# Kernel optimization log

Measured on AMD Instinct MI355X. Metric: run time of the kernel, lower is better.

Reference implementation:

```python
import jax, jax.numpy as jnp
import numpy as np

B, NUM_VN, NUM_CN, D = 4, 65536, 32768, 32
DEG = 8
E = NUM_CN * DEG  # 262144 edges per side
HID, MSG = 40, 20


def setup_inputs() -> dict:
    key = jax.random.key(0)
    ks = jax.random.split(key, 16)
    inp = {
        "h_from": jax.random.normal(ks[0], (B, NUM_VN, D), jnp.float32),
        "h_to_x": jax.random.normal(ks[1], (B, NUM_CN, D), jnp.float32),
        "h_to_z": jax.random.normal(ks[2], (B, NUM_CN, D), jnp.float32),
        "hx_logit": jax.random.normal(ks[3], (B, NUM_CN), jnp.float32),
        "hz_logit": jax.random.normal(ks[4], (B, NUM_CN), jnp.float32),
        "from_ind_x": jax.random.randint(ks[5], (E,), 0, NUM_VN, jnp.int32),
        "to_ind_x": jax.random.randint(ks[6], (E,), 0, NUM_CN, jnp.int32),
        "from_ind_z": jax.random.randint(ks[7], (E,), 0, NUM_VN, jnp.int32),
        "to_ind_z": jax.random.randint(ks[8], (E,), 0, NUM_CN, jnp.int32),
        # msg MLP: in 2*D -> HID -> MSG ; embed MLP: in MSG+D+1 -> HID -> D
        "Wm1_x": jax.random.normal(ks[9], (2 * D, HID), jnp.float32) * 0.1,
        "Wm2_x": jax.random.normal(ks[10], (HID, MSG), jnp.float32) * 0.1,
        "Wm1_z": jax.random.normal(ks[11], (2 * D, HID), jnp.float32) * 0.1,
        "Wm2_z": jax.random.normal(ks[12], (HID, MSG), jnp.float32) * 0.1,
        "We1_x": jax.random.normal(ks[13], (MSG + D + 1, HID), jnp.float32) * 0.1,
        "We2_x": jax.random.normal(ks[14], (HID, D), jnp.float32) * 0.1,
        "We1_z": jax.random.normal(ks[15], (MSG + D + 1, HID), jnp.float32) * 0.1,
        "We2_z": jax.random.normal(jax.random.fold_in(key, 99), (HID, D), jnp.float32) * 0.1,
    }
    return inp


def _side(h_from, h_to, logit, from_ind, to_ind, Wm1, Wm2, We1, We2):
    # gather edge endpoint embeddings: [B, E, 2*D]
    feat = jnp.concatenate([h_from[:, from_ind], h_to[:, to_ind]], axis=-1)
    # per-edge message MLP (relu hidden, linear out, no bias): [B, E, MSG]
    msg = jax.nn.relu(feat @ Wm1) @ Wm2
    # segment-sum aggregation onto receiving check nodes: [B, NUM_CN, MSG]
    n_cn = h_to.shape[1]
    m = jnp.zeros((h_to.shape[0], n_cn, msg.shape[-1]), msg.dtype).at[:, to_ind].add(msg)
    # embedding update MLP on [m, h_to, logit]: [B, NUM_CN, D]
    emb_in = jnp.concatenate([m, h_to, logit[..., None]], axis=-1)
    return jax.nn.relu(emb_in @ We1) @ We2


def reference(h_from, h_to_x, h_to_z, hx_logit, hz_logit,
              from_ind_x, to_ind_x, from_ind_z, to_ind_z,
              Wm1_x, Wm2_x, Wm1_z, Wm2_z, We1_x, We2_x, We1_z, We2_z):
    h_to_x_new = _side(h_from, h_to_x, hx_logit, from_ind_x, to_ind_x,
                       Wm1_x, Wm2_x, We1_x, We2_x)
    h_to_z_new = _side(h_from, h_to_z, hz_logit, from_ind_z, to_ind_z,
                       Wm1_z, Wm2_z, We1_z, We2_z)
    return (h_to_x_new, h_to_z_new)
```

## Files before the change

### kernel.cpp

```cpp
#include <hip/hip_runtime.h>

#define NVN 65536
#define NCN 32768
#define NB 4
#define DIM 32
#define NE 262144
#define HID 40
#define MSGD 20
#define SLOT 40

typedef unsigned short u16;
typedef unsigned int u32;
typedef __attribute__((ext_vector_type(8))) short bf16x8;
typedef __attribute__((ext_vector_type(4))) float f32x4;

__device__ __forceinline__ u16 f2bf(float f) {
    u32 u = __float_as_uint(f);
    u += 0x7fff + ((u >> 16) & 1);
    return (u16)(u >> 16);
}
__device__ __forceinline__ float bflo(u32 u) { return __uint_as_float(u << 16); }
__device__ __forceinline__ float bfhi(u32 u) { return __uint_as_float(u & 0xffff0000u); }
__device__ __forceinline__ u32 pk2(float a, float b) {
    return (u32)f2bf(a) | ((u32)f2bf(b) << 16);
}


__global__ __launch_bounds__(256) void scatter_slot(const int* __restrict__ to_x,
                                                    const int* __restrict__ from_x,
                                                    const int* __restrict__ to_z,
                                                    const int* __restrict__ from_z,
                                                    int* __restrict__ cnt_x,
                                                    int* __restrict__ cnt_z,
                                                    u16* __restrict__ ef_x,
                                                    u16* __restrict__ ef_z) {
    int bid = blockIdx.x;
    int e = (bid & 1023) * 256 + threadIdx.x;
    const int* t; const int* f; int* cnt; u16* ef;
    if (bid < 1024) { t = to_x; f = from_x; cnt = cnt_x; ef = ef_x; }
    else            { t = to_z; f = from_z; cnt = cnt_z; ef = ef_z; }
    int c = t[e];
    int pos = atomicAdd(&cnt[c], 1);
    if (pos < SLOT) ef[c * SLOT + pos] = (u16)f[e];
}


__global__ __launch_bounds__(256) void precomp_mfma(
        const float* __restrict__ h_x, const float* __restrict__ h_z,
        const float* __restrict__ W_x, const float* __restrict__ W_z,
        u16* __restrict__ dst_x, u16* __restrict__ dst_z,
        int nrows) {
    __shared__ __attribute__((aligned(16))) u16 sA[128 * 32];
    __shared__ __attribute__((aligned(16))) u16 sB[32 * 48];
    __shared__ __attribute__((aligned(16))) u16 sOut[128 * 40];

    int bps = nrows >> 5;
    int bid = blockIdx.x;
    int side = bid / bps;
    int v0 = (bid - side * bps) << 5;

    const float* __restrict__ h = side ? h_z : h_x;
    const float* __restrict__ W = side ? W_z : W_x;
    u16* dst = side ? dst_z : dst_x;

    int tid = threadIdx.x;

    for (int i = tid; i < 32 * 48; i += 256) {
        int row = i / 48, col = i - row * 48;
        sB[i] = (col < 40) ? f2bf(W[row * 40 + col]) : (u16)0;
    }
    {
        int r = tid >> 1, p = tid & 1;
        int b = r >> 5, vloc = r & 31;
        const float4* hp = (const float4*)(h + ((size_t)b * nrows + v0 + vloc) * DIM + p * 16);
        float4 x0 = hp[0], x1 = hp[1], x2 = hp[2], x3 = hp[3];
        uint4* d = (uint4*)(sA + r * 32 + p * 16);
        d[0] = make_uint4(pk2(x0.x, x0.y), pk2(x0.z, x0.w), pk2(x1.x, x1.y), pk2(x1.z, x1.w));
        d[1] = make_uint4(pk2(x2.x, x2.y), pk2(x2.z, x2.w), pk2(x3.x, x3.y), pk2(x3.z, x3.w));
    }
    __syncthreads();

    int wid = tid >> 6;
    int lane = tid & 63;
    int li = lane & 15;
    int lk = lane >> 4;

    bf16x8 bfr[3];
#pragma unroll
    for (int jt = 0; jt < 3; jt++) {
        bf16x8 v;
#pragma unroll
        for (int rr = 0; rr < 8; rr++)
            v[rr] = (short)sB[(lk * 8 + rr) * 48 + jt * 16 + li];
        bfr[jt] = v;
    }

#pragma unroll
    for (int rt = 0; rt < 2; rt++) {
        int rowloc = wid * 32 + rt * 16;
        bf16x8 a = *(const bf16x8*)(sA + (rowloc + li) * 32 + lk * 8);
#pragma unroll
        for (int jt = 0; jt < 3; jt++) {
            f32x4 acc = {0.f, 0.f, 0.f, 0.f};
            acc = __builtin_amdgcn_mfma_f32_16x16x32_bf16(a, bfr[jt], acc, 0, 0, 0);
            int col = jt * 16 + li;
            if (col < 40) {
#pragma unroll
                for (int rr = 0; rr < 4; rr++)
                    sOut[(rowloc + lk * 4 + rr) * 40 + col] = f2bf(acc[rr]);
            }
        }
    }
    __syncthreads();

    {
        const u32* so = (const u32*)sOut;
        uint4* dp = (uint4*)((char*)dst + (size_t)v0 * 320);
        for (int i = tid; i < 640; i += 256) {
            int vloc = i / 20;
            int q0 = (i - vloc * 20) * 4;
            u32 vals[4];
#pragma unroll
            for (int j = 0; j < 4; j++) {
                int q = q0 + j;
                int ch, cp;
                if (q < 32)      { ch = q >> 2;        cp = (ch >> 2) * 10 + (q & 3); }
                else if (q < 64) { int t = q - 32; ch = t >> 2; cp = (ch >> 2) * 10 + 4 + (t & 3); }
                else             { int t = q - 64; ch = t >> 1; cp = (ch >> 2) * 10 + 8 + (t & 1); }
                int m = (ch & 3) * 32 + vloc;
                vals[j] = so[m * 20 + cp];
            }
            dp[i] = make_uint4(vals[0], vals[1], vals[2], vals[3]);
        }
    }
}


__global__ __launch_bounds__(256) void prepW(
        const float* __restrict__ Wm2_x, const float* __restrict__ Wm2_z,
        const float* __restrict__ We1_x, const float* __restrict__ We1_z,
        const float* __restrict__ We2_x, const float* __restrict__ We2_z,
        u16* __restrict__ BW_x, u16* __restrict__ BW_z,
        u16* __restrict__ W2_x, u16* __restrict__ W2_z) {
    int side = blockIdx.x;
    const float* Wm2 = side ? Wm2_z : Wm2_x;
    const float* We1 = side ? We1_z : We1_x;
    const float* We2 = side ? We2_z : We2_x;
    u16* BW = side ? BW_z : BW_x;
    u16* W2 = side ? W2_z : W2_x;
    int tid = threadIdx.x;
    for (int i = tid; i < 96 * 48; i += 256) {
        int row = i / 48, col = i % 48;
        float v = 0.f;
        if (col < 40) {
            if (row < 40) {
                for (int k = 0; k < MSGD; k++) v += Wm2[row * MSGD + k] * We1[k * HID + col];
            } else if (row < 72) {
                v = We1[(MSGD + row - 40) * HID + col];
            } else if (row == 72) {
                v = We1[(MSGD + DIM) * HID + col];
            }
        }
        BW[i] = f2bf(v);
    }
    for (int i = tid; i < 64 * 32; i += 256) {
        int row = i / 32, col = i % 32;
        W2[i] = (row < 40) ? f2bf(We2[row * 32 + col]) : (u16)0;
    }
}


__global__ __launch_bounds__(256, 8) void aggA_kernel(
        const u16* __restrict__ U2h_x, const u16* __restrict__ U2h_z,
        u16* __restrict__ ts_x, u16* __restrict__ ts_z,
        const int* __restrict__ cnt_x, const int* __restrict__ cnt_z,
        const u16* __restrict__ ef_x, const u16* __restrict__ ef_z) {
    int side = blockIdx.x >> 10;
    const char* Ubase = (const char*)(side ? U2h_z : U2h_x);
    char* ts = (char*)(side ? ts_z : ts_x);
    const int* cnt = side ? cnt_z : cnt_x;
    const u16* ef = side ? ef_z : ef_x;

    int gt = (blockIdx.x & 1023) * 256 + threadIdx.x;
    int c = gt >> 3;
    int l8 = gt & 7;
    int off16a = l8 * 16;
    int off8c = 256 + l8 * 8;

    char* tline = ts + (size_t)c * 320;
    uint4 T0 = *(const uint4*)(tline + off16a);
    uint4 T1 = *(const uint4*)(tline + off16a + 128);
    uint2 Tc = *(const uint2*)(tline + off8c);

    float s[20];
#pragma unroll
    for (int k = 0; k < 20; k++) s[k] = 0.f;

    int cn = cnt[c];
    cn = (cn < SLOT) ? cn : SLOT;
    const u16* efc = ef + c * SLOT;

    int vA = (cn > 0) ? (int)efc[0] : 0;
#define ACC(su, aw, tw) { \
    s[su]     += fmaxf(bflo(aw) + bflo(tw), 0.f); \
    s[(su)+1] += fmaxf(bfhi(aw) + bfhi(tw), 0.f); }
    for (int i = 0; i < cn; ++i) {
        const char* pa = Ubase + (size_t)vA * 320;
        uint4 A0 = *(const uint4*)(pa + off16a);
        uint4 A1 = *(const uint4*)(pa + off16a + 128);
        uint2 A2 = *(const uint2*)(pa + off8c);
        vA = (i + 1 < cn) ? (int)efc[i + 1] : 0;
        ACC(0, A0.x, T0.x)  ACC(2, A0.y, T0.y)  ACC(4, A0.z, T0.z)  ACC(6, A0.w, T0.w)
        ACC(8, A1.x, T1.x)  ACC(10, A1.y, T1.y) ACC(12, A1.z, T1.z) ACC(14, A1.w, T1.w)
        ACC(16, A2.x, Tc.x) ACC(18, A2.y, Tc.y)
    }
#undef ACC

    u32 sp[10];
#pragma unroll
    for (int jq = 0; jq < 5; jq++) {
        sp[2 * jq]     = pk2(s[4 * jq + 0], s[4 * jq + 1]);
        sp[2 * jq + 1] = pk2(s[4 * jq + 2], s[4 * jq + 3]);
    }
    *(uint4*)(tline + off16a)       = make_uint4(sp[0], sp[1], sp[2], sp[3]);
    *(uint4*)(tline + off16a + 128) = make_uint4(sp[4], sp[5], sp[6], sp[7]);
    *(uint2*)(tline + off8c)        = make_uint2(sp[8], sp[9]);
}


__global__ __launch_bounds__(256) void aggB_mfma(
        const u16* __restrict__ ts_x, const u16* __restrict__ ts_z,
        const float* __restrict__ h_to_x, const float* __restrict__ h_to_z,
        const float* __restrict__ logit_x, const float* __restrict__ logit_z,
        const u16* __restrict__ BW_x, const u16* __restrict__ BW_z,
        const u16* __restrict__ W2_x, const u16* __restrict__ W2_z,
        float* __restrict__ out) {
    __shared__ __attribute__((aligned(16))) u16 sA[128 * 96];
    __shared__ __attribute__((aligned(16))) u16 sH[128 * 64];
    __shared__ __attribute__((aligned(16))) u16 sBW[96 * 48];
    __shared__ __attribute__((aligned(16))) u16 sW2[64 * 32];

    int bid = blockIdx.x;
    int side = bid >> 10;
    const u16* ts = side ? ts_z : ts_x;
    const float* h_to = side ? h_to_z : h_to_x;
    const float* logit = side ? logit_z : logit_x;
    const u16* BWg = side ? BW_z : BW_x;
    const u16* W2g = side ? W2_z : W2_x;

    int tid = threadIdx.x;
    int rho0 = (bid & 1023) * 128;
    int b = rho0 >> 15;
    int c0 = rho0 & 32767;

    for (int i = tid; i < (96 * 48) / 8; i += 256)
        ((uint4*)sBW)[i] = ((const uint4*)BWg)[i];
    if (tid < (64 * 32) / 8) ((uint4*)sW2)[tid] = ((const uint4*)W2g)[tid];

    {
        int r = tid >> 1;
        int part = tid & 1;
        int c = c0 + r;
        char* srow = (char*)sA + r * 192;
        if (part == 0) {
            const char* tr = (const char*)ts + (size_t)c * 320;
            uint4 p0 = *(const uint4*)(tr + b * 16);
            uint4 p1 = *(const uint4*)(tr + 128 + b * 16);
            uint2 p2 = *(const uint2*)(tr + 256 + b * 8);
            uint4 p3 = *(const uint4*)(tr + (4 + b) * 16);
            uint4 p4 = *(const uint4*)(tr + 128 + (4 + b) * 16);
            uint2 p5 = *(const uint2*)(tr + 256 + (4 + b) * 8);
            *(uint4*)(srow + 0)  = p0;
            *(uint4*)(srow + 16) = p1;
            *(uint2*)(srow + 32) = p2;
            *(uint2*)(srow + 40) = make_uint2(p3.x, p3.y);
            *(uint2*)(srow + 48) = make_uint2(p3.z, p3.w);
            *(uint2*)(srow + 56) = make_uint2(p4.x, p4.y);
            *(uint2*)(srow + 64) = make_uint2(p4.z, p4.w);
            *(uint2*)(srow + 72) = p5;
            char* hrow = (char*)sH + r * 128;
            *(uint4*)(hrow + 96)  = make_uint4(0, 0, 0, 0);
            *(uint4*)(hrow + 112) = make_uint4(0, 0, 0, 0);
        } else {
            const float4* xp = (const float4*)(h_to + ((size_t)b * NCN + c) * DIM);
#pragma unroll
            for (int q = 0; q < 4; q++) {
                float4 x0 = xp[2 * q], x1 = xp[2 * q + 1];
                *(uint4*)(srow + 80 + q * 16) =
                    make_uint4(pk2(x0.x, x0.y), pk2(x0.z, x0.w),
                               pk2(x1.x, x1.y), pk2(x1.z, x1.w));
            }
            float lg = logit[(size_t)b * NCN + c];
            *(uint4*)(srow + 144) = make_uint4((u32)f2bf(lg), 0, 0, 0);
            *(uint4*)(srow + 160) = make_uint4(0, 0, 0, 0);
            *(uint4*)(srow + 176) = make_uint4(0, 0, 0, 0);
        }
    }
    __syncthreads();

    int wid = tid >> 6;
    int lane = tid & 63;
    int li = lane & 15;
    int lk = lane >> 4;
    int rowq = lk * 4;

    bf16x8 bA[3][3];
#pragma unroll
    for (int jt = 0; jt < 3; jt++)
#pragma unroll
        for (int ks = 0; ks < 3; ks++) {
            bf16x8 v;
#pragma unroll
            for (int rr = 0; rr < 8; rr++)
                v[rr] = (short)sBW[(ks * 32 + lk * 8 + rr) * 48 + jt * 16 + li];
            bA[jt][ks] = v;
        }

#pragma unroll
    for (int rt = 0; rt < 2; rt++) {
        int rowloc = wid * 32 + rt * 16;
        const char* abase = (const char*)sA + (rowloc + li) * 192 + lk * 16;
        bf16x8 a0 = *(const bf16x8*)(abase);
        bf16x8 a1 = *(const bf16x8*)(abase + 64);
        bf16x8 a2 = *(const bf16x8*)(abase + 128);
#pragma unroll
        for (int jt = 0; jt < 3; jt++) {
            f32x4 acc = {0.f, 0.f, 0.f, 0.f};
            acc = __builtin_amdgcn_mfma_f32_16x16x32_bf16(a0, bA[jt][0], acc, 0, 0, 0);
            acc = __builtin_amdgcn_mfma_f32_16x16x32_bf16(a1, bA[jt][1], acc, 0, 0, 0);
            acc = __builtin_amdgcn_mfma_f32_16x16x32_bf16(a2, bA[jt][2], acc, 0, 0, 0);
#pragma unroll
            for (int rr = 0; rr < 4; rr++)
                sH[(rowloc + rowq + rr) * 64 + jt * 16 + li] = f2bf(fmaxf(acc[rr], 0.f));
        }
    }
    __syncthreads();

    bf16x8 bB[2][2];
#pragma unroll
    for (int jt = 0; jt < 2; jt++)
#pragma unroll
        for (int ks = 0; ks < 2; ks++) {
            bf16x8 v;
#pragma unroll
            for (int rr = 0; rr < 8; rr++)
                v[rr] = (short)sW2[(ks * 32 + lk * 8 + rr) * 32 + jt * 16 + li];
            bB[jt][ks] = v;
        }

    size_t rowg0 = (size_t)bid * 128;
#pragma unroll
    for (int rt = 0; rt < 2; rt++) {
        int rowloc = wid * 32 + rt * 16;
        const char* hbase = (const char*)sH + (rowloc + li) * 128 + lk * 16;
        bf16x8 h0 = *(const bf16x8*)(hbase);
        bf16x8 h1 = *(const bf16x8*)(hbase + 64);
#pragma unroll
        for (int jt = 0; jt < 2; jt++) {
            f32x4 acc = {0.f, 0.f, 0.f, 0.f};
            acc = __builtin_amdgcn_mfma_f32_16x16x32_bf16(h0, bB[jt][0], acc, 0, 0, 0);
            acc = __builtin_amdgcn_mfma_f32_16x16x32_bf16(h1, bB[jt][1], acc, 0, 0, 0);
#pragma unroll
            for (int rr = 0; rr < 4; rr++)
                out[(rowg0 + rowloc + rowq + rr) * 32 + jt * 16 + li] = acc[rr];
        }
    }
}


extern "C" void kernel_launch(void* const* d_in, const int* in_sizes, int n_in,
                              void* d_out, int out_size, void* d_ws, size_t ws_size,
                              hipStream_t stream) {
    const float* h_from   = (const float*)d_in[0];
    const float* h_to_x   = (const float*)d_in[1];
    const float* h_to_z   = (const float*)d_in[2];
    const float* hx_logit = (const float*)d_in[3];
    const float* hz_logit = (const float*)d_in[4];
    const int*   from_x   = (const int*)d_in[5];
    const int*   to_x     = (const int*)d_in[6];
    const int*   from_z   = (const int*)d_in[7];
    const int*   to_z     = (const int*)d_in[8];
    const float* Wm1_x    = (const float*)d_in[9];
    const float* Wm2_x    = (const float*)d_in[10];
    const float* Wm1_z    = (const float*)d_in[11];
    const float* Wm2_z    = (const float*)d_in[12];
    const float* We1_x    = (const float*)d_in[13];
    const float* We2_x    = (const float*)d_in[14];
    const float* We1_z    = (const float*)d_in[15];
    const float* We2_z    = (const float*)d_in[16];

    char* ws = (char*)d_ws;
    u16* U2h_x = (u16*)(ws);
    u16* U2h_z = (u16*)(ws + 20971520);
    u16* ts_x  = (u16*)(ws + 41943040);
    u16* ts_z  = (u16*)(ws + 52428800);
    u16* ef_x  = (u16*)(ws + 62914560);
    u16* ef_z  = (u16*)(ws + 65536000);
    int* cnt_x = (int*)(ws + 68157440);
    int* cnt_z = (int*)(ws + 68288512);
    u16* BW_x  = (u16*)(ws + 68419584);
    u16* BW_z  = (u16*)(ws + 68428800);
    u16* W2_x  = (u16*)(ws + 68438016);
    u16* W2_z  = (u16*)(ws + 68442112);
    float* out = (float*)d_out;

    hipMemsetAsync(ws + 68157440, 0, 262144, stream);
    scatter_slot<<<2048, 256, 0, stream>>>(to_x, from_x, to_z, from_z,
                                           cnt_x, cnt_z, ef_x, ef_z);
    precomp_mfma<<<4096, 256, 0, stream>>>(h_from, h_from, Wm1_x, Wm1_z,
                                           U2h_x, U2h_z, NVN);
    precomp_mfma<<<2048, 256, 0, stream>>>(h_to_x, h_to_z,
                                           Wm1_x + DIM * HID, Wm1_z + DIM * HID,
                                           ts_x, ts_z, NCN);
    prepW<<<2, 256, 0, stream>>>(Wm2_x, Wm2_z, We1_x, We1_z, We2_x, We2_z,
                                 BW_x, BW_z, W2_x, W2_z);
    aggA_kernel<<<2048, 256, 0, stream>>>(U2h_x, U2h_z, ts_x, ts_z,
                                          cnt_x, cnt_z, ef_x, ef_z);
    aggB_mfma<<<2048, 256, 0, stream>>>(ts_x, ts_z, h_to_x, h_to_z,
                                        hx_logit, hz_logit,
                                        BW_x, BW_z, W2_x, W2_z, out);
}
```

Before: 146.8 us.

## Merge setup kernels into one launch and split aggA edges across two lanes

Four independent setup kernels (slot scatter, two precomputation GEMMs, weight prep) are merged into a single launch dispatched by block-index range, so their launch gaps and tails overlap. The gather-aggregation kernel now uses 16 threads per check node instead of 8; each half walks alternating edges and the partial sums are combined with a cross-lane shuffle. This doubles memory-level parallelism on the irregular gather. In exchange, the merged kernel carries the largest shared-memory footprint for every block, and the shuffle reduction adds a little work.

```diff
diff --git a/kernel.cpp b/kernel.cpp
--- a/kernel.cpp
+++ b/kernel.cpp
@@ -26,44 +26,19 @@
 }
 
 
-__global__ __launch_bounds__(256) void scatter_slot(const int* __restrict__ to_x,
-                                                    const int* __restrict__ from_x,
-                                                    const int* __restrict__ to_z,
-                                                    const int* __restrict__ from_z,
-                                                    int* __restrict__ cnt_x,
-                                                    int* __restrict__ cnt_z,
-                                                    u16* __restrict__ ef_x,
-                                                    u16* __restrict__ ef_z) {
-    int bid = blockIdx.x;
-    int e = (bid & 1023) * 256 + threadIdx.x;
-    const int* t; const int* f; int* cnt; u16* ef;
-    if (bid < 1024) { t = to_x; f = from_x; cnt = cnt_x; ef = ef_x; }
-    else            { t = to_z; f = from_z; cnt = cnt_z; ef = ef_z; }
-    int c = t[e];
-    int pos = atomicAdd(&cnt[c], 1);
-    if (pos < SLOT) ef[c * SLOT + pos] = (u16)f[e];
-}
-
-
-__global__ __launch_bounds__(256) void precomp_mfma(
+__device__ __forceinline__ void precomp_body(
+        int bidl, int tid,
         const float* __restrict__ h_x, const float* __restrict__ h_z,
         const float* __restrict__ W_x, const float* __restrict__ W_z,
-        u16* __restrict__ dst_x, u16* __restrict__ dst_z,
-        int nrows) {
-    __shared__ __attribute__((aligned(16))) u16 sA[128 * 32];
-    __shared__ __attribute__((aligned(16))) u16 sB[32 * 48];
-    __shared__ __attribute__((aligned(16))) u16 sOut[128 * 40];
-
+        u16* __restrict__ dst_x, u16* __restrict__ dst_z, int nrows,
+        u16* sA, u16* sB, u16* sOut) {
     int bps = nrows >> 5;
-    int bid = blockIdx.x;
-    int side = bid / bps;
-    int v0 = (bid - side * bps) << 5;
+    int side = bidl / bps;
+    int v0 = (bidl - side * bps) << 5;
 
     const float* __restrict__ h = side ? h_z : h_x;
     const float* __restrict__ W = side ? W_z : W_x;
     u16* dst = side ? dst_z : dst_x;
-
-    int tid = threadIdx.x;
 
     for (int i = tid; i < 32 * 48; i += 256) {
         int row = i / 48, col = i - row * 48;
@@ -136,36 +111,68 @@
 }
 
 
-__global__ __launch_bounds__(256) void prepW(
+__global__ __launch_bounds__(256) void phase1(
+        const int* __restrict__ to_x, const int* __restrict__ from_x,
+        const int* __restrict__ to_z, const int* __restrict__ from_z,
+        int* __restrict__ cnt_x, int* __restrict__ cnt_z,
+        u16* __restrict__ ef_x, u16* __restrict__ ef_z,
+        const float* __restrict__ h_from,
+        const float* __restrict__ h_to_x, const float* __restrict__ h_to_z,
+        const float* __restrict__ Wm1_x, const float* __restrict__ Wm1_z,
         const float* __restrict__ Wm2_x, const float* __restrict__ Wm2_z,
         const float* __restrict__ We1_x, const float* __restrict__ We1_z,
         const float* __restrict__ We2_x, const float* __restrict__ We2_z,
+        u16* __restrict__ U2h_x, u16* __restrict__ U2h_z,
+        u16* __restrict__ ts_x, u16* __restrict__ ts_z,
         u16* __restrict__ BW_x, u16* __restrict__ BW_z,
         u16* __restrict__ W2_x, u16* __restrict__ W2_z) {
-    int side = blockIdx.x;
-    const float* Wm2 = side ? Wm2_z : Wm2_x;
-    const float* We1 = side ? We1_z : We1_x;
-    const float* We2 = side ? We2_z : We2_x;
-    u16* BW = side ? BW_z : BW_x;
-    u16* W2 = side ? W2_z : W2_x;
+    __shared__ __attribute__((aligned(16))) u16 sA[128 * 32];
+    __shared__ __attribute__((aligned(16))) u16 sB[32 * 48];
+    __shared__ __attribute__((aligned(16))) u16 sOut[128 * 40];
+
+    int bid = blockIdx.x;
     int tid = threadIdx.x;
-    for (int i = tid; i < 96 * 48; i += 256) {
-        int row = i / 48, col = i % 48;
-        float v = 0.f;
-        if (col < 40) {
-            if (row < 40) {
-                for (int k = 0; k < MSGD; k++) v += Wm2[row * MSGD + k] * We1[k * HID + col];
-            } else if (row < 72) {
-                v = We1[(MSGD + row - 40) * HID + col];
-            } else if (row == 72) {
-                v = We1[(MSGD + DIM) * HID + col];
+
+    if (bid < 2048) {
+        int e = (bid & 1023) * 256 + tid;
+        const int* t; const int* f; int* cnt; u16* ef;
+        if (bid < 1024) { t = to_x; f = from_x; cnt = cnt_x; ef = ef_x; }
+        else            { t = to_z; f = from_z; cnt = cnt_z; ef = ef_z; }
+        int c = t[e];
+        int pos = atomicAdd(&cnt[c], 1);
+        if (pos < SLOT) ef[c * SLOT + pos] = (u16)f[e];
+    } else if (bid < 6144) {
+        precomp_body(bid - 2048, tid, h_from, h_from, Wm1_x, Wm1_z,
+                     U2h_x, U2h_z, NVN, sA, sB, sOut);
+    } else if (bid < 8192) {
+        precomp_body(bid - 6144, tid, h_to_x, h_to_z,
+                     Wm1_x + DIM * HID, Wm1_z + DIM * HID,
+                     ts_x, ts_z, NCN, sA, sB, sOut);
+    } else {
+        int side = bid - 8192;
+        const float* Wm2 = side ? Wm2_z : Wm2_x;
+        const float* We1 = side ? We1_z : We1_x;
+        const float* We2 = side ? We2_z : We2_x;
+        u16* BW = side ? BW_z : BW_x;
+        u16* W2 = side ? W2_z : W2_x;
+        for (int i = tid; i < 96 * 48; i += 256) {
+            int row = i / 48, col = i % 48;
+            float v = 0.f;
+            if (col < 40) {
+                if (row < 40) {
+                    for (int k = 0; k < MSGD; k++) v += Wm2[row * MSGD + k] * We1[k * HID + col];
+                } else if (row < 72) {
+                    v = We1[(MSGD + row - 40) * HID + col];
+                } else if (row == 72) {
+                    v = We1[(MSGD + DIM) * HID + col];
+                }
             }
-        }
-        BW[i] = f2bf(v);
-    }
-    for (int i = tid; i < 64 * 32; i += 256) {
-        int row = i / 32, col = i % 32;
-        W2[i] = (row < 40) ? f2bf(We2[row * 32 + col]) : (u16)0;
+            BW[i] = f2bf(v);
+        }
+        for (int i = tid; i < 64 * 32; i += 256) {
+            int row = i / 32, col = i % 32;
+            W2[i] = (row < 40) ? f2bf(We2[row * 32 + col]) : (u16)0;
+        }
     }
 }
 
@@ -175,17 +182,19 @@
         u16* __restrict__ ts_x, u16* __restrict__ ts_z,
         const int* __restrict__ cnt_x, const int* __restrict__ cnt_z,
         const u16* __restrict__ ef_x, const u16* __restrict__ ef_z) {
-    int side = blockIdx.x >> 10;
+    int side = blockIdx.x >> 11;
     const char* Ubase = (const char*)(side ? U2h_z : U2h_x);
     char* ts = (char*)(side ? ts_z : ts_x);
     const int* cnt = side ? cnt_z : cnt_x;
     const u16* ef = side ? ef_z : ef_x;
 
-    int gt = (blockIdx.x & 1023) * 256 + threadIdx.x;
-    int c = gt >> 3;
-    int l8 = gt & 7;
-    int off16a = l8 * 16;
-    int off8c = 256 + l8 * 8;
+    int gt = (blockIdx.x & 2047) * 256 + threadIdx.x;
+    int c = gt >> 4;
+    int l16 = gt & 15;
+    int chunk = l16 & 7;
+    int par = l16 >> 3;
+    int off16a = chunk * 16;
+    int off8c = 256 + chunk * 8;
 
     char* tline = ts + (size_t)c * 320;
     uint4 T0 = *(const uint4*)(tline + off16a);
@@ -200,31 +209,36 @@
     cn = (cn < SLOT) ? cn : SLOT;
     const u16* efc = ef + c * SLOT;
 
-    int vA = (cn > 0) ? (int)efc[0] : 0;
+    int vA = (par < cn) ? (int)efc[par] : 0;
 #define ACC(su, aw, tw) { \
     s[su]     += fmaxf(bflo(aw) + bflo(tw), 0.f); \
     s[(su)+1] += fmaxf(bfhi(aw) + bfhi(tw), 0.f); }
-    for (int i = 0; i < cn; ++i) {
+    for (int i = par; i < cn; i += 2) {
         const char* pa = Ubase + (size_t)vA * 320;
         uint4 A0 = *(const uint4*)(pa + off16a);
         uint4 A1 = *(const uint4*)(pa + off16a + 128);
         uint2 A2 = *(const uint2*)(pa + off8c);
-        vA = (i + 1 < cn) ? (int)efc[i + 1] : 0;
+        vA = (i + 2 < cn) ? (int)efc[i + 2] : 0;
         ACC(0, A0.x, T0.x)  ACC(2, A0.y, T0.y)  ACC(4, A0.z, T0.z)  ACC(6, A0.w, T0.w)
         ACC(8, A1.x, T1.x)  ACC(10, A1.y, T1.y) ACC(12, A1.z, T1.z) ACC(14, A1.w, T1.w)
         ACC(16, A2.x, Tc.x) ACC(18, A2.y, Tc.y)
     }
 #undef ACC
 
-    u32 sp[10];
-#pragma unroll
-    for (int jq = 0; jq < 5; jq++) {
-        sp[2 * jq]     = pk2(s[4 * jq + 0], s[4 * jq + 1]);
-        sp[2 * jq + 1] = pk2(s[4 * jq + 2], s[4 * jq + 3]);
-    }
-    *(uint4*)(tline + off16a)       = make_uint4(sp[0], sp[1], sp[2], sp[3]);
-    *(uint4*)(tline + off16a + 128) = make_uint4(sp[4], sp[5], sp[6], sp[7]);
-    *(uint2*)(tline + off8c)        = make_uint2(sp[8], sp[9]);
+#pragma unroll
+    for (int k = 0; k < 20; k++) s[k] += __shfl_xor(s[k], 8);
+
+    if (par == 0) {
+        u32 sp[10];
+#pragma unroll
+        for (int jq = 0; jq < 5; jq++) {
+            sp[2 * jq]     = pk2(s[4 * jq + 0], s[4 * jq + 1]);
+            sp[2 * jq + 1] = pk2(s[4 * jq + 2], s[4 * jq + 3]);
+        }
+        *(uint4*)(tline + off16a)       = make_uint4(sp[0], sp[1], sp[2], sp[3]);
+        *(uint4*)(tline + off16a + 128) = make_uint4(sp[4], sp[5], sp[6], sp[7]);
+        *(uint2*)(tline + off8c)        = make_uint2(sp[8], sp[9]);
+    }
 }
 
 
@@ -405,16 +419,14 @@
     float* out = (float*)d_out;
 
     hipMemsetAsync(ws + 68157440, 0, 262144, stream);
-    scatter_slot<<<2048, 256, 0, stream>>>(to_x, from_x, to_z, from_z,
-                                           cnt_x, cnt_z, ef_x, ef_z);
-    precomp_mfma<<<4096, 256, 0, stream>>>(h_from, h_from, Wm1_x, Wm1_z,
-                                           U2h_x, U2h_z, NVN);
-    precomp_mfma<<<2048, 256, 0, stream>>>(h_to_x, h_to_z,
-                                           Wm1_x + DIM * HID, Wm1_z + DIM * HID,
-                                           ts_x, ts_z, NCN);
-    prepW<<<2, 256, 0, stream>>>(Wm2_x, Wm2_z, We1_x, We1_z, We2_x, We2_z,
-                                 BW_x, BW_z, W2_x, W2_z);
-    aggA_kernel<<<2048, 256, 0, stream>>>(U2h_x, U2h_z, ts_x, ts_z,
+    phase1<<<8194, 256, 0, stream>>>(to_x, from_x, to_z, from_z,
+                                     cnt_x, cnt_z, ef_x, ef_z,
+                                     h_from, h_to_x, h_to_z,
+                                     Wm1_x, Wm1_z, Wm2_x, Wm2_z,
+                                     We1_x, We1_z, We2_x, We2_z,
+                                     U2h_x, U2h_z, ts_x, ts_z,
+                                     BW_x, BW_z, W2_x, W2_z);
+    aggA_kernel<<<4096, 256, 0, stream>>>(U2h_x, U2h_z, ts_x, ts_z,
                                           cnt_x, cnt_z, ef_x, ef_z);
     aggB_mfma<<<2048, 256, 0, stream>>>(ts_x, ts_z, h_to_x, h_to_z,
                                         hx_logit, hz_logit,
```

Measured after the change: 131.2 us. 1.12x faster.
